# Kernel tuning notes

Hardware: AMD Instinct MI355X
Metric: run time of the kernel (lower is better)

Reference implementation:

```python
import jax, jax.numpy as jnp
import numpy as np
from jax import lax


def setup_inputs() -> dict:
    key = jax.random.key(0)
    k1, k2 = jax.random.split(key)
    B, C, N, K = 8, 1024, 8192, 3
    x = jax.random.normal(k1, (B, C, N), dtype=jnp.float32)
    filt = jax.random.normal(k2, (C, K), dtype=jnp.float32)
    return {"x": x, "filter": filt}


def reference(x, filter):
    # Depthwise (per-channel) 1D valid cross-correlation:
    # out[b, c, i] = sum_k x[b, c, i + k] * filter[c, k]
    # (Winograd transform is an algorithmic detail; math equals direct conv.)
    B, C, N = x.shape
    K = filter.shape[1]
    kernel = filter[:, None, :]  # (C, 1, K) -> OIH with feature_group_count=C
    out = lax.conv_general_dilated(
        x, kernel,
        window_strides=(1,),
        padding='VALID',
        dimension_numbers=('NCH', 'OIH', 'NCH'),
        feature_group_count=C,
    )  # (B, C, N - K + 1)
    return out
```

## Files before the change

### kernel.cpp

```cpp
#include <hip/hip_runtime.h>
#include <hip/hip_bf16.h>


#define C_DIM 1024
#define N_IN 8192
#define N_OUT 8190

__global__ __launch_bounds__(256) void dwconv1d_k3_kernel(
    const float* __restrict__ x,
    const float* __restrict__ filt,
    float* __restrict__ out)
{
    const int row = blockIdx.x;
    const int c = row & (C_DIM - 1);

    const float f0 = filt[c * 3 + 0];
    const float f1 = filt[c * 3 + 1];
    const float f2 = filt[c * 3 + 2];

    const float* __restrict__ xr = x + (size_t)row * N_IN;
    float* __restrict__ orow = out + (size_t)row * N_OUT;

    for (int g = threadIdx.x; g < 2048; g += 256) {
        const int n = g * 4;
        const float4 a = *reinterpret_cast<const float4*>(xr + n);
        if (g < 2047) {
            const float2 b = *reinterpret_cast<const float2*>(xr + n + 4);
            float2 lo, hi;
            lo.x = a.x * f0 + a.y * f1 + a.z * f2;
            lo.y = a.y * f0 + a.z * f1 + a.w * f2;
            hi.x = a.z * f0 + a.w * f1 + b.x * f2;
            hi.y = a.w * f0 + b.x * f1 + b.y * f2;
            *reinterpret_cast<float2*>(orow + n)     = lo;
            *reinterpret_cast<float2*>(orow + n + 2) = hi;
        } else {
            float2 lo;
            lo.x = a.x * f0 + a.y * f1 + a.z * f2;
            lo.y = a.y * f0 + a.z * f1 + a.w * f2;
            *reinterpret_cast<float2*>(orow + n) = lo;
        }
    }
}

extern "C" void kernel_launch(void* const* d_in, const int* in_sizes, int n_in,
                              void* d_out, int out_size, void* d_ws, size_t ws_size,
                              hipStream_t stream) {
    const float* x    = (const float*)d_in[0];
    const float* filt = (const float*)d_in[1];
    float* out        = (float*)d_out;

    const int rows = 8 * C_DIM;
    dwconv1d_k3_kernel<<<rows, 256, 0, stream>>>(x, filt, out);
}
```

Before: 104.7 us.

## Use 16-byte aligned output stores per row parity with batched loads and nontemporal writes

```diff
diff --git a/kernel.cpp b/kernel.cpp
--- a/kernel.cpp
+++ b/kernel.cpp
@@ -6,6 +6,9 @@
 #define N_IN 8192
 #define N_OUT 8190
 
+typedef float vfloat4 __attribute__((ext_vector_type(4)));
+typedef float vfloat2 __attribute__((ext_vector_type(2)));
+
 __global__ __launch_bounds__(256) void dwconv1d_k3_kernel(
     const float* __restrict__ x,
     const float* __restrict__ filt,
@@ -13,6 +16,7 @@
 {
     const int row = blockIdx.x;
     const int c = row & (C_DIM - 1);
+    const int tid = threadIdx.x;
 
     const float f0 = filt[c * 3 + 0];
     const float f1 = filt[c * 3 + 1];
@@ -21,23 +25,62 @@
     const float* __restrict__ xr = x + (size_t)row * N_IN;
     float* __restrict__ orow = out + (size_t)row * N_OUT;
 
-    for (int g = threadIdx.x; g < 2048; g += 256) {
-        const int n = g * 4;
-        const float4 a = *reinterpret_cast<const float4*>(xr + n);
-        if (g < 2047) {
-            const float2 b = *reinterpret_cast<const float2*>(xr + n + 4);
-            float2 lo, hi;
-            lo.x = a.x * f0 + a.y * f1 + a.z * f2;
-            lo.y = a.y * f0 + a.z * f1 + a.w * f2;
-            hi.x = a.z * f0 + a.w * f1 + b.x * f2;
-            hi.y = a.w * f0 + b.x * f1 + b.y * f2;
-            *reinterpret_cast<float2*>(orow + n)     = lo;
-            *reinterpret_cast<float2*>(orow + n + 2) = hi;
-        } else {
-            float2 lo;
-            lo.x = a.x * f0 + a.y * f1 + a.z * f2;
-            lo.y = a.y * f0 + a.z * f1 + a.w * f2;
-            *reinterpret_cast<float2*>(orow + n) = lo;
+    vfloat4 a[8];
+    vfloat2 b[8];
+
+    if ((row & 1) == 0) {
+        #pragma unroll
+        for (int p = 0; p < 8; ++p) {
+            int g = p * 256 + tid;
+            g = (g > 2046) ? 2046 : g;
+            const int n = g * 4;
+            a[p] = *reinterpret_cast<const vfloat4*>(xr + n);
+            b[p] = *reinterpret_cast<const vfloat2*>(xr + n + 4);
+        }
+        #pragma unroll
+        for (int p = 0; p < 8; ++p) {
+            const int g = p * 256 + tid;
+            vfloat4 o;
+            o.x = a[p].x * f0 + a[p].y * f1 + a[p].z * f2;
+            o.y = a[p].y * f0 + a[p].z * f1 + a[p].w * f2;
+            o.z = a[p].z * f0 + a[p].w * f1 + b[p].x * f2;
+            o.w = a[p].w * f0 + b[p].x * f1 + b[p].y * f2;
+            if (g < 2047)
+                __builtin_nontemporal_store(o, reinterpret_cast<vfloat4*>(orow + g * 4));
+        }
+        if (tid == 0) {
+            const vfloat4 t4 = *reinterpret_cast<const vfloat4*>(xr + 8188);
+            vfloat2 t;
+            t.x = t4.x * f0 + t4.y * f1 + t4.z * f2;
+            t.y = t4.y * f0 + t4.z * f1 + t4.w * f2;
+            __builtin_nontemporal_store(t, reinterpret_cast<vfloat2*>(orow + 8188));
+        }
+    } else {
+        #pragma unroll
+        for (int p = 0; p < 8; ++p) {
+            int g = p * 256 + tid;
+            g = (g > 2046) ? 2046 : g;
+            const int n = g * 4;
+            b[p] = *reinterpret_cast<const vfloat2*>(xr + n + 2);
+            a[p] = *reinterpret_cast<const vfloat4*>(xr + n + 4);
+        }
+        #pragma unroll
+        for (int p = 0; p < 8; ++p) {
+            const int g = p * 256 + tid;
+            vfloat4 o;
+            o.x = b[p].x * f0 + b[p].y * f1 + a[p].x * f2;
+            o.y = b[p].y * f0 + a[p].x * f1 + a[p].y * f2;
+            o.z = a[p].x * f0 + a[p].y * f1 + a[p].z * f2;
+            o.w = a[p].y * f0 + a[p].z * f1 + a[p].w * f2;
+            if (g < 2047)
+                __builtin_nontemporal_store(o, reinterpret_cast<vfloat4*>(orow + g * 4 + 2));
+        }
+        if (tid == 0) {
+            const vfloat4 h4 = *reinterpret_cast<const vfloat4*>(xr);
+            vfloat2 h;
+            h.x = h4.x * f0 + h4.y * f1 + h4.z * f2;
+            h.y = h4.y * f0 + h4.z * f1 + h4.w * f2;
+            __builtin_nontemporal_store(h, reinterpret_cast<vfloat2*>(orow));
         }
     }
 }
```

New measurement: 85.97 us. -17.9%, faster.
